# Kernel tuning notes

Hardware: AMD Instinct MI355X
Metric: run time of the kernel (lower is better)

Reference implementation:

```python
import jax, jax.numpy as jnp
import numpy as np

N_SRC = 50000
N_DST = 50000
E = 800000
SRC_DIM = 128
DST_DIM = 128
OUT_DIM = 128
HEADS = 4
D_HEAD = OUT_DIM // HEADS  # 32, concat=True


def setup_inputs() -> dict:
    key = jax.random.key(0)
    ks = jax.random.split(key, 10)
    x_src = jax.random.normal(ks[0], (N_SRC, SRC_DIM), dtype=jnp.float32)
    x_dst = jax.random.normal(ks[1], (N_DST, DST_DIM), dtype=jnp.float32)
    edge_src = jax.random.randint(ks[2], (E,), 0, N_SRC)
    edge_dst = jax.random.randint(ks[3], (E,), 0, N_DST)
    # parameters (torch Linear stored as [in, out] so y = x @ W)
    W_src = jax.random.normal(ks[4], (SRC_DIM, HEADS * D_HEAD), dtype=jnp.float32) / np.sqrt(SRC_DIM)
    W_dst = jax.random.normal(ks[5], (DST_DIM, HEADS * D_HEAD), dtype=jnp.float32) / np.sqrt(DST_DIM)
    att_src = jax.random.normal(ks[6], (1, HEADS, D_HEAD), dtype=jnp.float32) * 0.01
    att_dst = jax.random.normal(ks[7], (1, HEADS, D_HEAD), dtype=jnp.float32) * 0.01
    W_self = jax.random.normal(ks[8], (DST_DIM, HEADS * D_HEAD), dtype=jnp.float32) / np.sqrt(DST_DIM)
    b_self = jax.random.normal(ks[9], (HEADS * D_HEAD,), dtype=jnp.float32) * 0.01
    return {
        "x_src": x_src, "x_dst": x_dst,
        "edge_src": edge_src, "edge_dst": edge_dst, "num_dst": N_DST,
        "W_src": W_src, "W_dst": W_dst,
        "att_src": att_src, "att_dst": att_dst,
        "W_self": W_self, "b_self": b_self,
    }


def reference(x_src, x_dst, edge_src, edge_dst, num_dst,
              W_src, W_dst, att_src, att_dst, W_self, b_self):
    H, D = HEADS, D_HEAD
    src_feat = (x_src @ W_src).reshape(-1, H, D)   # [N_src, H, D]
    dst_feat = (x_dst @ W_dst).reshape(-1, H, D)   # [N_dst, H, D]

    src_edge = src_feat[edge_src]                   # [E, H, D] gather
    dst_edge = dst_feat[edge_dst]                   # [E, H, D] gather

    alpha_src = jnp.sum(src_edge * att_src, axis=-1)  # [E, H]
    alpha_dst = jnp.sum(dst_edge * att_dst, axis=-1)  # [E, H]
    alpha = jax.nn.leaky_relu(alpha_src + alpha_dst, negative_slope=0.2)

    # segment softmax over edges grouped by destination node
    a_max = jax.ops.segment_max(alpha, edge_dst, num_segments=num_dst)  # [N_dst, H]
    alpha = jnp.exp(alpha - a_max[edge_dst])
    a_sum = jax.ops.segment_sum(alpha, edge_dst, num_segments=num_dst)  # [N_dst, H]
    alpha = alpha / (a_sum[edge_dst] + 1e-16)

    msg = (src_edge * alpha[..., None]).reshape(-1, H * D)  # [E, H*D]
    agg = jax.ops.segment_sum(msg, edge_dst, num_segments=num_dst)  # [N_dst, H*D]

    return agg + x_dst @ W_self + b_self
```

## Files before the change

kernel.cpp:

```cpp
#include <hip/hip_runtime.h>

#define N_SRC 50000
#define N_DST 50000
#define NE    800000
#define DIM   128
#define HEADS 4

typedef short short8 __attribute__((ext_vector_type(8)));
typedef float f32x4 __attribute__((ext_vector_type(4)));

__device__ __forceinline__ float bf2f(unsigned short u) {
  union { unsigned int i; float f; } v;
  v.i = ((unsigned int)u) << 16;
  return v.f;
}

__device__ __forceinline__ unsigned short f2bf(float f) {
  unsigned int u = __float_as_uint(f);
  u += 0x7fffu + ((u >> 16) & 1u);
  return (unsigned short)(u >> 16);
}

__global__ void prep_kernel(const float* __restrict__ Wsrc, const float* __restrict__ Wself,
                            const float* __restrict__ Wdst,
                            const float* __restrict__ att_s, const float* __restrict__ att_d,
                            unsigned short* __restrict__ Wt_src,
                            unsigned short* __restrict__ Wt_self,
                            float* __restrict__ wt_s, float* __restrict__ wt_d) {
  const int b = blockIdx.x, t = threadIdx.x;
  if (b == 0) {
    for (int idx = t; idx < DIM * DIM; idx += 256) {
      int k = idx >> 7, n = idx & 127;
      Wt_src[n * DIM + k] = f2bf(Wsrc[idx]);
    }
  } else if (b == 1) {
    for (int idx = t; idx < DIM * DIM; idx += 256) {
      int k = idx >> 7, n = idx & 127;
      Wt_self[n * DIM + k] = f2bf(Wself[idx]);
    }
  } else {
    for (int i = t; i < 512; i += 256) {
      int k = i >> 2, h = i & 3;
      float ss = 0.f, sd = 0.f;
#pragma unroll 8
      for (int d = 0; d < 32; d++) {
        ss += Wsrc[k * DIM + h * 32 + d] * att_s[h * 32 + d];
        sd += Wdst[k * DIM + h * 32 + d] * att_d[h * 32 + d];
      }
      wt_s[h * DIM + k] = ss;
      wt_d[h * DIM + k] = sd;
    }
  }
}

__global__ __launch_bounds__(256) void mfma_src_kernel(
    const float* __restrict__ x, const unsigned short* __restrict__ Wt,
    const float* __restrict__ wt,
    unsigned short* __restrict__ feat, float* __restrict__ as_) {
  const int wave = threadIdx.x >> 6;
  const int lane = threadIdx.x & 63;
  const int r0 = (blockIdx.x * 4 + wave) * 16;
  const int rowa = lane & 15;
  const int kg = lane >> 4;

  f32x4 acc[8];
#pragma unroll
  for (int n = 0; n < 8; n++) acc[n] = (f32x4){0.f, 0.f, 0.f, 0.f};
  float p[4] = {0.f, 0.f, 0.f, 0.f};

  int rA = r0 + rowa;
  if (rA >= N_SRC) rA = N_SRC - 1;

#pragma unroll
  for (int ks = 0; ks < 4; ks++) {
    const int k = ks * 32 + kg * 8;
    const float4 xa = *(const float4*)&x[rA * DIM + k];
    const float4 xb = *(const float4*)&x[rA * DIM + k + 4];
#pragma unroll
    for (int h = 0; h < 4; h++) {
      const float4 wa = *(const float4*)&wt[h * DIM + k];
      const float4 wb = *(const float4*)&wt[h * DIM + k + 4];
      p[h] += xa.x * wa.x + xa.y * wa.y + xa.z * wa.z + xa.w * wa.w +
              xb.x * wb.x + xb.y * wb.y + xb.z * wb.z + xb.w * wb.w;
    }
    short8 af;
    af[0] = (short)f2bf(xa.x); af[1] = (short)f2bf(xa.y);
    af[2] = (short)f2bf(xa.z); af[3] = (short)f2bf(xa.w);
    af[4] = (short)f2bf(xb.x); af[5] = (short)f2bf(xb.y);
    af[6] = (short)f2bf(xb.z); af[7] = (short)f2bf(xb.w);
#pragma unroll
    for (int n = 0; n < 8; n++) {
      const short8 bf = *(const short8*)&Wt[(n * 16 + rowa) * DIM + k];
      acc[n] = __builtin_amdgcn_mfma_f32_16x16x32_bf16(af, bf, acc[n], 0, 0, 0);
    }
  }

  const int rowd = kg * 4;
#pragma unroll
  for (int n = 0; n < 8; n++) {
#pragma unroll
    for (int r = 0; r < 4; r++) {
      const int row = r0 + rowd + r;
      if (row < N_SRC) feat[row * DIM + n * 16 + rowa] = f2bf(acc[n][r]);
    }
  }

#pragma unroll
  for (int h = 0; h < 4; h++) {
    p[h] += __shfl_xor(p[h], 16);
    p[h] += __shfl_xor(p[h], 32);
  }
  if (lane < 16 && r0 + lane < N_SRC) {
    *(float4*)&as_[(r0 + lane) * 4] = make_float4(p[0], p[1], p[2], p[3]);
  }
}

__global__ __launch_bounds__(256) void mfma_dst_kernel(
    const float* __restrict__ x, const unsigned short* __restrict__ Wt,
    const float* __restrict__ wt, const float* __restrict__ bias,
    float* __restrict__ out, float* __restrict__ ad_) {
  const int wave = threadIdx.x >> 6;
  const int lane = threadIdx.x & 63;
  const int r0 = (blockIdx.x * 4 + wave) * 16;
  const int rowa = lane & 15;
  const int kg = lane >> 4;

  f32x4 acc[8];
#pragma unroll
  for (int n = 0; n < 8; n++) acc[n] = (f32x4){0.f, 0.f, 0.f, 0.f};
  float p[4] = {0.f, 0.f, 0.f, 0.f};

  int rA = r0 + rowa;
  if (rA >= N_DST) rA = N_DST - 1;

#pragma unroll
  for (int ks = 0; ks < 4; ks++) {
    const int k = ks * 32 + kg * 8;
    const float4 xa = *(const float4*)&x[rA * DIM + k];
    const float4 xb = *(const float4*)&x[rA * DIM + k + 4];
#pragma unroll
    for (int h = 0; h < 4; h++) {
      const float4 wa = *(const float4*)&wt[h * DIM + k];
      const float4 wb = *(const float4*)&wt[h * DIM + k + 4];
      p[h] += xa.x * wa.x + xa.y * wa.y + xa.z * wa.z + xa.w * wa.w +
              xb.x * wb.x + xb.y * wb.y + xb.z * wb.z + xb.w * wb.w;
    }
    short8 af;
    af[0] = (short)f2bf(xa.x); af[1] = (short)f2bf(xa.y);
    af[2] = (short)f2bf(xa.z); af[3] = (short)f2bf(xa.w);
    af[4] = (short)f2bf(xb.x); af[5] = (short)f2bf(xb.y);
    af[6] = (short)f2bf(xb.z); af[7] = (short)f2bf(xb.w);
#pragma unroll
    for (int n = 0; n < 8; n++) {
      const short8 bf = *(const short8*)&Wt[(n * 16 + rowa) * DIM + k];
      acc[n] = __builtin_amdgcn_mfma_f32_16x16x32_bf16(af, bf, acc[n], 0, 0, 0);
    }
  }

  const int rowd = kg * 4;
#pragma unroll
  for (int n = 0; n < 8; n++) {
    const float b = bias[n * 16 + rowa];
#pragma unroll
    for (int r = 0; r < 4; r++) {
      const int row = r0 + rowd + r;
      if (row < N_DST) out[row * DIM + n * 16 + rowa] = acc[n][r] + b;
    }
  }

#pragma unroll
  for (int h = 0; h < 4; h++) {
    p[h] += __shfl_xor(p[h], 16);
    p[h] += __shfl_xor(p[h], 32);
  }
  if (lane < 16 && r0 + lane < N_DST) {
    *(float4*)&ad_[(r0 + lane) * 4] = make_float4(p[0], p[1], p[2], p[3]);
  }
}

__global__ void hist_kernel(const int* __restrict__ edst, int* __restrict__ deg) {
  int e = blockIdx.x * 256 + threadIdx.x;
  if (e < NE) atomicAdd(&deg[edst[e]], 1);
}

__global__ void scan1_kernel(const int* __restrict__ deg, int* __restrict__ offs,
                             int* __restrict__ bsum, int n) {
  __shared__ int sh[256];
  int i = blockIdx.x * 256 + threadIdx.x;
  int v = (i < n) ? deg[i] : 0;
  sh[threadIdx.x] = v;
  __syncthreads();
  for (int d = 1; d < 256; d <<= 1) {
    int tv = (threadIdx.x >= d) ? sh[threadIdx.x - d] : 0;
    __syncthreads();
    sh[threadIdx.x] += tv;
    __syncthreads();
  }
  if (i < n) offs[i] = sh[threadIdx.x] - v;
  if (threadIdx.x == 255) bsum[blockIdx.x] = sh[255];
}

__global__ void scan2_kernel(int* __restrict__ bsum, int n) {
  __shared__ int sh[256];
  int v = (threadIdx.x < n) ? bsum[threadIdx.x] : 0;
  sh[threadIdx.x] = v;
  __syncthreads();
  for (int d = 1; d < 256; d <<= 1) {
    int tv = (threadIdx.x >= d) ? sh[threadIdx.x - d] : 0;
    __syncthreads();
    sh[threadIdx.x] += tv;
    __syncthreads();
  }
  if (threadIdx.x < n) bsum[threadIdx.x] = sh[threadIdx.x] - v;
}

__global__ void fill_kernel(const int* __restrict__ esrc, const int* __restrict__ edst,
                            const float* __restrict__ as_, const float* __restrict__ ad_,
                            const int* __restrict__ offs, const int* __restrict__ bsum,
                            int* __restrict__ cursor,
                            int* __restrict__ csr_src, float4* __restrict__ csr_alpha) {
  int e = blockIdx.x * 256 + threadIdx.x;
  if (e >= NE) return;
  int s = esrc[e], d = edst[e];
  int p = atomicAdd(&cursor[d], 1);
  int slot = offs[d] + bsum[d >> 8] + p;
  csr_src[slot] = s;
  const float4 av = *(const float4*)&as_[s * 4];
  const float4 bv = *(const float4*)&ad_[d * 4];
  float4 a;
  a.x = av.x + bv.x; a.y = av.y + bv.y; a.z = av.z + bv.z; a.w = av.w + bv.w;
  a.x = a.x > 0.f ? a.x : 0.2f * a.x;
  a.y = a.y > 0.f ? a.y : 0.2f * a.y;
  a.z = a.z > 0.f ? a.z : 0.2f * a.z;
  a.w = a.w > 0.f ? a.w : 0.2f * a.w;
  csr_alpha[slot] = a;
}

__global__ __launch_bounds__(256) void agg_kernel(
    const unsigned short* __restrict__ feat, const int* __restrict__ csr_src,
    const float* __restrict__ csr_alpha, const int* __restrict__ offs,
    const int* __restrict__ bsum, const int* __restrict__ deg,
    float* __restrict__ out) {
  const int wave = threadIdx.x >> 6;
  const int lane = threadIdx.x & 63;
  const int n = blockIdx.x * 4 + wave;
  if (n >= N_DST) return;
  const int beg = offs[n] + bsum[n >> 8];
  const int end = beg + deg[n];
  const int sub = lane >> 5;
  const int lp = lane & 31;
  const int h = lp >> 3;

  float4 o = make_float4(0.f, 0.f, 0.f, 0.f);
  if (sub == 0) o = *(const float4*)&out[n * DIM + lp * 4];

  float s = 0.f;
  float a0 = 0.f, a1 = 0.f, a2 = 0.f, a3 = 0.f;

  int k = beg + sub;
  int sid = 0;
  float a = -1e30f;
  if (k < end) {
    sid = csr_src[k];
    a = csr_alpha[k * 4 + h];
  }
  while (k < end) {
    int k2 = k + 2;
    int sid2 = 0;
    float an = -1e30f;
    if (k2 < end) {
      sid2 = csr_src[k2];
      an = csr_alpha[k2 * 4 + h];
    }
    float w = __expf(a);
    ushort4 f = *(const ushort4*)&feat[sid * DIM + lp * 4];
    s += w;
    a0 += w * bf2f(f.x);
    a1 += w * bf2f(f.y);
    a2 += w * bf2f(f.z);
    a3 += w * bf2f(f.w);
    k = k2;
    sid = sid2;
    a = an;
  }

  s += __shfl_xor(s, 32);
  a0 += __shfl_xor(a0, 32);
  a1 += __shfl_xor(a1, 32);
  a2 += __shfl_xor(a2, 32);
  a3 += __shfl_xor(a3, 32);

  if (sub == 0) {
    const float inv = 1.f / (s + 1e-16f);
    o.x += a0 * inv;
    o.y += a1 * inv;
    o.z += a2 * inv;
    o.w += a3 * inv;
    *(float4*)&out[n * DIM + lp * 4] = o;
  }
}

extern "C" void kernel_launch(void* const* d_in, const int* in_sizes, int n_in,
                              void* d_out, int out_size, void* d_ws, size_t ws_size,
                              hipStream_t stream) {
  const float* x_src  = (const float*)d_in[0];
  const float* x_dst  = (const float*)d_in[1];
  const int*   esrc   = (const int*)d_in[2];
  const int*   edst   = (const int*)d_in[3];
  const float* W_src  = (const float*)d_in[5];
  const float* W_dst  = (const float*)d_in[6];
  const float* att_s  = (const float*)d_in[7];
  const float* att_d  = (const float*)d_in[8];
  const float* W_self = (const float*)d_in[9];
  const float* b_self = (const float*)d_in[10];
  float* out = (float*)d_out;

  char* ws = (char*)d_ws;
  size_t off = 0;
  auto carve = [&](size_t bytes) {
    void* p = ws + off;
    off += (bytes + 255) & ~size_t(255);
    return p;
  };
  unsigned short* feat   = (unsigned short*)carve(sizeof(unsigned short) * N_SRC * DIM);
  float* as_   = (float*)carve(sizeof(float) * N_SRC * HEADS);
  float* ad_   = (float*)carve(sizeof(float) * N_DST * HEADS);
  int* deg     = (int*)carve(sizeof(int) * N_DST);
  int* cursor  = (int*)carve(sizeof(int) * N_DST);
  int* offs    = (int*)carve(sizeof(int) * N_DST);
  int* bsum    = (int*)carve(sizeof(int) * 256);
  int* csr_src = (int*)carve(sizeof(int) * NE);
  float4* csr_alpha = (float4*)carve(sizeof(float4) * NE);
  unsigned short* Wt_src  = (unsigned short*)carve(sizeof(unsigned short) * DIM * DIM);
  unsigned short* Wt_self = (unsigned short*)carve(sizeof(unsigned short) * DIM * DIM);
  float* wt_s = (float*)carve(sizeof(float) * HEADS * DIM);
  float* wt_d = (float*)carve(sizeof(float) * HEADS * DIM);
  (void)ws_size;

  hipMemsetAsync(deg, 0, sizeof(int) * N_DST, stream);
  hipMemsetAsync(cursor, 0, sizeof(int) * N_DST, stream);

  prep_kernel<<<3, 256, 0, stream>>>(W_src, W_self, W_dst, att_s, att_d,
                                     Wt_src, Wt_self, wt_s, wt_d);
  hist_kernel<<<(NE + 255) / 256, 256, 0, stream>>>(edst, deg);

  const int gemm_blocks = (N_SRC + 63) / 64;
  mfma_src_kernel<<<gemm_blocks, 256, 0, stream>>>(x_src, Wt_src, wt_s, feat, as_);
  mfma_dst_kernel<<<gemm_blocks, 256, 0, stream>>>(x_dst, Wt_self, wt_d, b_self, out, ad_);

  const int nblk = (N_DST + 255) / 256;
  scan1_kernel<<<nblk, 256, 0, stream>>>(deg, offs, bsum, N_DST);
  scan2_kernel<<<1, 256, 0, stream>>>(bsum, nblk);
  fill_kernel<<<(NE + 255) / 256, 256, 0, stream>>>(esrc, edst, as_, ad_, offs, bsum, cursor,
                                                    csr_src, (float4*)csr_alpha);
  agg_kernel<<<(N_DST + 3) / 4, 256, 0, stream>>>(feat, csr_src, (const float*)csr_alpha,
                                                  offs, bsum, deg, out);
}
```

Baseline: 324.4 us.

## Fuse GEMMs with histogram, fold attention logits into MFMA, compute alpha in aggregation

```diff
diff --git a/kernel.cpp b/kernel.cpp
--- a/kernel.cpp
+++ b/kernel.cpp
@@ -5,6 +5,9 @@
 #define NE    800000
 #define DIM   128
 #define HEADS 4
+#define NB_GEMM 782
+#define NB_HIST 3125
+#define WROWS 144
 
 typedef short short8 __attribute__((ext_vector_type(8)));
 typedef float f32x4 __attribute__((ext_vector_type(4)));
@@ -21,166 +24,147 @@
   return (unsigned short)(u >> 16);
 }
 
-__global__ void prep_kernel(const float* __restrict__ Wsrc, const float* __restrict__ Wself,
-                            const float* __restrict__ Wdst,
-                            const float* __restrict__ att_s, const float* __restrict__ att_d,
-                            unsigned short* __restrict__ Wt_src,
-                            unsigned short* __restrict__ Wt_self,
-                            float* __restrict__ wt_s, float* __restrict__ wt_d) {
+__global__ void setup_kernel(const float* __restrict__ Wsrc, const float* __restrict__ Wself,
+                             const float* __restrict__ Wdst,
+                             const float* __restrict__ att_s, const float* __restrict__ att_d,
+                             unsigned short* __restrict__ Wps, unsigned short* __restrict__ Wpd,
+                             int* __restrict__ deg, int* __restrict__ cursor) {
   const int b = blockIdx.x, t = threadIdx.x;
   if (b == 0) {
-    for (int idx = t; idx < DIM * DIM; idx += 256) {
-      int k = idx >> 7, n = idx & 127;
-      Wt_src[n * DIM + k] = f2bf(Wsrc[idx]);
+    for (int i = t; i < DIM * DIM; i += 256) {
+      int k = i >> 7, n = i & 127;
+      Wps[n * DIM + k] = f2bf(Wsrc[i]);
     }
   } else if (b == 1) {
-    for (int idx = t; idx < DIM * DIM; idx += 256) {
-      int k = idx >> 7, n = idx & 127;
-      Wt_self[n * DIM + k] = f2bf(Wself[idx]);
+    for (int i = t; i < DIM * DIM; i += 256) {
+      int k = i >> 7, n = i & 127;
+      Wpd[n * DIM + k] = f2bf(Wself[i]);
+    }
+  } else if (b == 2) {
+    for (int i = t; i < 2 * 4 * DIM; i += 256) {
+      int which = (i >= 4 * DIM) ? 1 : 0;
+      int j = which ? i - 4 * DIM : i;
+      int h = j >> 7, k = j & 127;
+      const float* W = which ? Wdst : Wsrc;
+      const float* att = which ? att_d : att_s;
+      float s = 0.f;
+#pragma unroll 8
+      for (int d = 0; d < 32; d++) s += W[k * DIM + h * 32 + d] * att[h * 32 + d];
+      (which ? Wpd : Wps)[(128 + h) * DIM + k] = f2bf(s);
+    }
+    for (int i = t; i < 2 * 12 * DIM; i += 256) {
+      int which = (i >= 12 * DIM) ? 1 : 0;
+      int j = which ? i - 12 * DIM : i;
+      (which ? Wpd : Wps)[132 * DIM + j] = 0;
     }
   } else {
-    for (int i = t; i < 512; i += 256) {
-      int k = i >> 2, h = i & 3;
-      float ss = 0.f, sd = 0.f;
-#pragma unroll 8
-      for (int d = 0; d < 32; d++) {
-        ss += Wsrc[k * DIM + h * 32 + d] * att_s[h * 32 + d];
-        sd += Wdst[k * DIM + h * 32 + d] * att_d[h * 32 + d];
+    int i = (b - 3) * 1024 + t * 4;
+    int4 z = make_int4(0, 0, 0, 0);
+    if (i < N_DST) *(int4*)&deg[i] = z;
+    else {
+      int j = i - N_DST;
+      if (j < N_DST) *(int4*)&cursor[j] = z;
+    }
+  }
+}
+
+__global__ __launch_bounds__(256) void phase1_kernel(
+    const float* __restrict__ x_src, const float* __restrict__ x_dst,
+    const unsigned short* __restrict__ Wps, const unsigned short* __restrict__ Wpd,
+    const int* __restrict__ edst,
+    unsigned short* __restrict__ feat, float* __restrict__ as_, float* __restrict__ ad_,
+    float* __restrict__ out, const float* __restrict__ bias, int* __restrict__ deg) {
+  __shared__ unsigned short lx[64 * DIM];
+  __shared__ unsigned short lw[WROWS * DIM];
+  const int b = blockIdx.x, t = threadIdx.x;
+
+  if (b >= 2 * NB_GEMM) {
+    int e = (b - 2 * NB_GEMM) * 256 + t;
+    if (e < NE) atomicAdd(&deg[edst[e]], 1);
+    return;
+  }
+
+  const bool is_dst = (b >= NB_GEMM);
+  const int blk = is_dst ? b - NB_GEMM : b;
+  const float* __restrict__ x = is_dst ? x_dst : x_src;
+  const unsigned short* __restrict__ Wp = is_dst ? Wpd : Wps;
+  const int r0 = blk * 64;
+
+  for (int c = t; c < WROWS * 16; c += 256) {
+    int row = c >> 4, slot = c & 15;
+    short8 v = *(const short8*)&Wp[row * DIM + slot * 8];
+    *(short8*)((char*)lw + row * 256 + ((slot ^ (row & 15)) << 4)) = v;
+  }
+  for (int c = t; c < 64 * 16; c += 256) {
+    int row = c >> 4, slot = c & 15;
+    int gr = r0 + row;
+    if (gr >= N_SRC) gr = N_SRC - 1;
+    const float4 va = *(const float4*)&x[gr * DIM + slot * 8];
+    const float4 vb = *(const float4*)&x[gr * DIM + slot * 8 + 4];
+    short8 v;
+    v[0] = (short)f2bf(va.x); v[1] = (short)f2bf(va.y);
+    v[2] = (short)f2bf(va.z); v[3] = (short)f2bf(va.w);
+    v[4] = (short)f2bf(vb.x); v[5] = (short)f2bf(vb.y);
+    v[6] = (short)f2bf(vb.z); v[7] = (short)f2bf(vb.w);
+    *(short8*)((char*)lx + row * 256 + ((slot ^ (row & 15)) << 4)) = v;
+  }
+  __syncthreads();
+
+  const int wave = t >> 6, lane = t & 63;
+  const int rowa = lane & 15, kg = lane >> 4;
+  const int xrow = wave * 16 + rowa;
+
+  f32x4 acc[9];
+#pragma unroll
+  for (int n = 0; n < 9; n++) acc[n] = (f32x4){0.f, 0.f, 0.f, 0.f};
+
+#pragma unroll
+  for (int ks = 0; ks < 4; ks++) {
+    const int slot = ks * 4 + kg;
+    const short8 af = *(const short8*)((char*)lx + xrow * 256 + ((slot ^ rowa) << 4));
+#pragma unroll
+    for (int n = 0; n < 9; n++) {
+      const int wr = n * 16 + rowa;
+      const short8 bf = *(const short8*)((char*)lw + wr * 256 + ((slot ^ rowa) << 4));
+      acc[n] = __builtin_amdgcn_mfma_f32_16x16x32_bf16(af, bf, acc[n], 0, 0, 0);
+    }
+  }
+
+  const int orow0 = r0 + wave * 16 + kg * 4;
+  if (!is_dst) {
+#pragma unroll
+    for (int n = 0; n < 8; n++) {
+#pragma unroll
+      for (int r = 0; r < 4; r++) {
+        int row = orow0 + r;
+        if (row < N_SRC) feat[row * DIM + n * 16 + rowa] = f2bf(acc[n][r]);
       }
-      wt_s[h * DIM + k] = ss;
-      wt_d[h * DIM + k] = sd;
-    }
-  }
-}
-
-__global__ __launch_bounds__(256) void mfma_src_kernel(
-    const float* __restrict__ x, const unsigned short* __restrict__ Wt,
-    const float* __restrict__ wt,
-    unsigned short* __restrict__ feat, float* __restrict__ as_) {
-  const int wave = threadIdx.x >> 6;
-  const int lane = threadIdx.x & 63;
-  const int r0 = (blockIdx.x * 4 + wave) * 16;
-  const int rowa = lane & 15;
-  const int kg = lane >> 4;
-
-  f32x4 acc[8];
-#pragma unroll
-  for (int n = 0; n < 8; n++) acc[n] = (f32x4){0.f, 0.f, 0.f, 0.f};
-  float p[4] = {0.f, 0.f, 0.f, 0.f};
-
-  int rA = r0 + rowa;
-  if (rA >= N_SRC) rA = N_SRC - 1;
-
-#pragma unroll
-  for (int ks = 0; ks < 4; ks++) {
-    const int k = ks * 32 + kg * 8;
-    const float4 xa = *(const float4*)&x[rA * DIM + k];
-    const float4 xb = *(const float4*)&x[rA * DIM + k + 4];
-#pragma unroll
-    for (int h = 0; h < 4; h++) {
-      const float4 wa = *(const float4*)&wt[h * DIM + k];
-      const float4 wb = *(const float4*)&wt[h * DIM + k + 4];
-      p[h] += xa.x * wa.x + xa.y * wa.y + xa.z * wa.z + xa.w * wa.w +
-              xb.x * wb.x + xb.y * wb.y + xb.z * wb.z + xb.w * wb.w;
-    }
-    short8 af;
-    af[0] = (short)f2bf(xa.x); af[1] = (short)f2bf(xa.y);
-    af[2] = (short)f2bf(xa.z); af[3] = (short)f2bf(xa.w);
-    af[4] = (short)f2bf(xb.x); af[5] = (short)f2bf(xb.y);
-    af[6] = (short)f2bf(xb.z); af[7] = (short)f2bf(xb.w);
+    }
+    if (rowa < HEADS) {
+#pragma unroll
+      for (int r = 0; r < 4; r++) {
+        int row = orow0 + r;
+        if (row < N_SRC) as_[row * HEADS + rowa] = acc[8][r];
+      }
+    }
+  } else {
 #pragma unroll
     for (int n = 0; n < 8; n++) {
-      const short8 bf = *(const short8*)&Wt[(n * 16 + rowa) * DIM + k];
-      acc[n] = __builtin_amdgcn_mfma_f32_16x16x32_bf16(af, bf, acc[n], 0, 0, 0);
-    }
-  }
-
-  const int rowd = kg * 4;
-#pragma unroll
-  for (int n = 0; n < 8; n++) {
-#pragma unroll
-    for (int r = 0; r < 4; r++) {
-      const int row = r0 + rowd + r;
-      if (row < N_SRC) feat[row * DIM + n * 16 + rowa] = f2bf(acc[n][r]);
-    }
-  }
-
-#pragma unroll
-  for (int h = 0; h < 4; h++) {
-    p[h] += __shfl_xor(p[h], 16);
-    p[h] += __shfl_xor(p[h], 32);
-  }
-  if (lane < 16 && r0 + lane < N_SRC) {
-    *(float4*)&as_[(r0 + lane) * 4] = make_float4(p[0], p[1], p[2], p[3]);
-  }
-}
-
-__global__ __launch_bounds__(256) void mfma_dst_kernel(
-    const float* __restrict__ x, const unsigned short* __restrict__ Wt,
-    const float* __restrict__ wt, const float* __restrict__ bias,
-    float* __restrict__ out, float* __restrict__ ad_) {
-  const int wave = threadIdx.x >> 6;
-  const int lane = threadIdx.x & 63;
-  const int r0 = (blockIdx.x * 4 + wave) * 16;
-  const int rowa = lane & 15;
-  const int kg = lane >> 4;
-
-  f32x4 acc[8];
-#pragma unroll
-  for (int n = 0; n < 8; n++) acc[n] = (f32x4){0.f, 0.f, 0.f, 0.f};
-  float p[4] = {0.f, 0.f, 0.f, 0.f};
-
-  int rA = r0 + rowa;
-  if (rA >= N_DST) rA = N_DST - 1;
-
-#pragma unroll
-  for (int ks = 0; ks < 4; ks++) {
-    const int k = ks * 32 + kg * 8;
-    const float4 xa = *(const float4*)&x[rA * DIM + k];
-    const float4 xb = *(const float4*)&x[rA * DIM + k + 4];
-#pragma unroll
-    for (int h = 0; h < 4; h++) {
-      const float4 wa = *(const float4*)&wt[h * DIM + k];
-      const float4 wb = *(const float4*)&wt[h * DIM + k + 4];
-      p[h] += xa.x * wa.x + xa.y * wa.y + xa.z * wa.z + xa.w * wa.w +
-              xb.x * wb.x + xb.y * wb.y + xb.z * wb.z + xb.w * wb.w;
-    }
-    short8 af;
-    af[0] = (short)f2bf(xa.x); af[1] = (short)f2bf(xa.y);
-    af[2] = (short)f2bf(xa.z); af[3] = (short)f2bf(xa.w);
-    af[4] = (short)f2bf(xb.x); af[5] = (short)f2bf(xb.y);
-    af[6] = (short)f2bf(xb.z); af[7] = (short)f2bf(xb.w);
-#pragma unroll
-    for (int n = 0; n < 8; n++) {
-      const short8 bf = *(const short8*)&Wt[(n * 16 + rowa) * DIM + k];
-      acc[n] = __builtin_amdgcn_mfma_f32_16x16x32_bf16(af, bf, acc[n], 0, 0, 0);
-    }
-  }
-
-  const int rowd = kg * 4;
-#pragma unroll
-  for (int n = 0; n < 8; n++) {
-    const float b = bias[n * 16 + rowa];
-#pragma unroll
-    for (int r = 0; r < 4; r++) {
-      const int row = r0 + rowd + r;
-      if (row < N_DST) out[row * DIM + n * 16 + rowa] = acc[n][r] + b;
-    }
-  }
-
-#pragma unroll
-  for (int h = 0; h < 4; h++) {
-    p[h] += __shfl_xor(p[h], 16);
-    p[h] += __shfl_xor(p[h], 32);
-  }
-  if (lane < 16 && r0 + lane < N_DST) {
-    *(float4*)&ad_[(r0 + lane) * 4] = make_float4(p[0], p[1], p[2], p[3]);
-  }
-}
-
-__global__ void hist_kernel(const int* __restrict__ edst, int* __restrict__ deg) {
-  int e = blockIdx.x * 256 + threadIdx.x;
-  if (e < NE) atomicAdd(&deg[edst[e]], 1);
+      const float bb = bias[n * 16 + rowa];
+#pragma unroll
+      for (int r = 0; r < 4; r++) {
+        int row = orow0 + r;
+        if (row < N_DST) out[row * DIM + n * 16 + rowa] = acc[n][r] + bb;
+      }
+    }
+    if (rowa < HEADS) {
+#pragma unroll
+      for (int r = 0; r < 4; r++) {
+        int row = orow0 + r;
+        if (row < N_DST) ad_[row * HEADS + rowa] = acc[8][r];
+      }
+    }
+  }
 }
 
 __global__ void scan1_kernel(const int* __restrict__ deg, int* __restrict__ offs,
@@ -215,88 +199,84 @@
 }
 
 __global__ void fill_kernel(const int* __restrict__ esrc, const int* __restrict__ edst,
-                            const float* __restrict__ as_, const float* __restrict__ ad_,
                             const int* __restrict__ offs, const int* __restrict__ bsum,
-                            int* __restrict__ cursor,
-                            int* __restrict__ csr_src, float4* __restrict__ csr_alpha) {
+                            int* __restrict__ cursor, int* __restrict__ csr_src) {
   int e = blockIdx.x * 256 + threadIdx.x;
   if (e >= NE) return;
   int s = esrc[e], d = edst[e];
   int p = atomicAdd(&cursor[d], 1);
-  int slot = offs[d] + bsum[d >> 8] + p;
-  csr_src[slot] = s;
-  const float4 av = *(const float4*)&as_[s * 4];
-  const float4 bv = *(const float4*)&ad_[d * 4];
-  float4 a;
-  a.x = av.x + bv.x; a.y = av.y + bv.y; a.z = av.z + bv.z; a.w = av.w + bv.w;
-  a.x = a.x > 0.f ? a.x : 0.2f * a.x;
-  a.y = a.y > 0.f ? a.y : 0.2f * a.y;
-  a.z = a.z > 0.f ? a.z : 0.2f * a.z;
-  a.w = a.w > 0.f ? a.w : 0.2f * a.w;
-  csr_alpha[slot] = a;
+  csr_src[offs[d] + bsum[d >> 8] + p] = s;
 }
 
 __global__ __launch_bounds__(256) void agg_kernel(
     const unsigned short* __restrict__ feat, const int* __restrict__ csr_src,
-    const float* __restrict__ csr_alpha, const int* __restrict__ offs,
-    const int* __restrict__ bsum, const int* __restrict__ deg,
-    float* __restrict__ out) {
+    const float* __restrict__ as_, const float* __restrict__ ad_,
+    const int* __restrict__ offs, const int* __restrict__ bsum,
+    const int* __restrict__ deg, float* __restrict__ out) {
   const int wave = threadIdx.x >> 6;
   const int lane = threadIdx.x & 63;
   const int n = blockIdx.x * 4 + wave;
   if (n >= N_DST) return;
+  const int g = lane >> 4, q = lane & 15;
+  const int h = q >> 2;
   const int beg = offs[n] + bsum[n >> 8];
   const int end = beg + deg[n];
-  const int sub = lane >> 5;
-  const int lp = lane & 31;
-  const int h = lp >> 3;
-
-  float4 o = make_float4(0.f, 0.f, 0.f, 0.f);
-  if (sub == 0) o = *(const float4*)&out[n * DIM + lp * 4];
+  const float adh = ad_[n * HEADS + h];
+
+  float4 oa, ob;
+  if (g == 0) {
+    oa = *(const float4*)&out[n * DIM + q * 8];
+    ob = *(const float4*)&out[n * DIM + q * 8 + 4];
+  }
 
   float s = 0.f;
-  float a0 = 0.f, a1 = 0.f, a2 = 0.f, a3 = 0.f;
-
-  int k = beg + sub;
+  float acc[8];
+#pragma unroll
+  for (int j = 0; j < 8; j++) acc[j] = 0.f;
+
+  int k = beg + g;
   int sid = 0;
-  float a = -1e30f;
+  float ash = -1e30f;
   if (k < end) {
     sid = csr_src[k];
-    a = csr_alpha[k * 4 + h];
+    ash = as_[sid * HEADS + h];
   }
   while (k < end) {
-    int k2 = k + 2;
-    int sid2 = 0;
-    float an = -1e30f;
-    if (k2 < end) {
-      sid2 = csr_src[k2];
-      an = csr_alpha[k2 * 4 + h];
-    }
-    float w = __expf(a);
-    ushort4 f = *(const ushort4*)&feat[sid * DIM + lp * 4];
+    const int kn = k + 4;
+    int sid_n = 0;
+    float ash_n = -1e30f;
+    if (kn < end) {
+      sid_n = csr_src[kn];
+      ash_n = as_[sid_n * HEADS + h];
+    }
+    float al = ash + adh;
+    al = al > 0.f ? al : 0.2f * al;
+    const float w = __expf(al);
+    const short8 f = *(const short8*)&feat[sid * DIM + q * 8];
     s += w;
-    a0 += w * bf2f(f.x);
-    a1 += w * bf2f(f.y);
-    a2 += w * bf2f(f.z);
-    a3 += w * bf2f(f.w);
-    k = k2;
-    sid = sid2;
-    a = an;
-  }
-
+#pragma unroll
+    for (int j = 0; j < 8; j++) acc[j] += w * bf2f((unsigned short)f[j]);
+    k = kn;
+    sid = sid_n;
+    ash = ash_n;
+  }
+
+  s += __shfl_xor(s, 16);
   s += __shfl_xor(s, 32);
-  a0 += __shfl_xor(a0, 32);
-  a1 += __shfl_xor(a1, 32);
-  a2 += __shfl_xor(a2, 32);
-  a3 += __shfl_xor(a3, 32);
-
-  if (sub == 0) {
+#pragma unroll
+  for (int j = 0; j < 8; j++) {
+    acc[j] += __shfl_xor(acc[j], 16);
+    acc[j] += __shfl_xor(acc[j], 32);
+  }
+
+  if (g == 0) {
     const float inv = 1.f / (s + 1e-16f);
-    o.x += a0 * inv;
-    o.y += a1 * inv;
-    o.z += a2 * inv;
-    o.w += a3 * inv;
-    *(float4*)&out[n * DIM + lp * 4] = o;
+    oa.x += acc[0] * inv; oa.y += acc[1] * inv;
+    oa.z += acc[2] * inv; oa.w += acc[3] * inv;
+    ob.x += acc[4] * inv; ob.y += acc[5] * inv;
+    ob.z += acc[6] * inv; ob.w += acc[7] * inv;
+    *(float4*)&out[n * DIM + q * 8] = oa;
+    *(float4*)&out[n * DIM + q * 8 + 4] = ob;
   }
 }
 
@@ -314,6 +294,7 @@
   const float* W_self = (const float*)d_in[9];
   const float* b_self = (const float*)d_in[10];
   float* out = (float*)d_out;
+  (void)in_sizes; (void)n_in; (void)out_size; (void)ws_size;
 
   char* ws = (char*)d_ws;
   size_t off = 0;
@@ -322,7 +303,7 @@
     off += (bytes + 255) & ~size_t(255);
     return p;
   };
-  unsigned short* feat   = (unsigned short*)carve(sizeof(unsigned short) * N_SRC * DIM);
+  unsigned short* feat = (unsigned short*)carve(sizeof(unsigned short) * N_SRC * DIM);
   float* as_   = (float*)carve(sizeof(float) * N_SRC * HEADS);
   float* ad_   = (float*)carve(sizeof(float) * N_DST * HEADS);
   int* deg     = (int*)carve(sizeof(int) * N_DST);
@@ -330,29 +311,17 @@
   int* offs    = (int*)carve(sizeof(int) * N_DST);
   int* bsum    = (int*)carve(sizeof(int) * 256);
   int* csr_src = (int*)carve(sizeof(int) * NE);
-  float4* csr_alpha = (float4*)carve(sizeof(float4) * NE);
-  unsigned short* Wt_src  = (unsigned short*)carve(sizeof(unsigned short) * DIM * DIM);
-  unsigned short* Wt_self = (unsigned short*)carve(sizeof(unsigned short) * DIM * DIM);
-  float* wt_s = (float*)carve(sizeof(float) * HEADS * DIM);
-  float* wt_d = (float*)carve(sizeof(float) * HEADS * DIM);
-  (void)ws_size;
-
-  hipMemsetAsync(deg, 0, sizeof(int) * N_DST, stream);
-  hipMemsetAsync(cursor, 0, sizeof(int) * N_DST, stream);
-
-  prep_kernel<<<3, 256, 0, stream>>>(W_src, W_self, W_dst, att_s, att_d,
-                                     Wt_src, Wt_self, wt_s, wt_d);
-  hist_kernel<<<(NE + 255) / 256, 256, 0, stream>>>(edst, deg);
-
-  const int gemm_blocks = (N_SRC + 63) / 64;
-  mfma_src_kernel<<<gemm_blocks, 256, 0, stream>>>(x_src, Wt_src, wt_s, feat, as_);
-  mfma_dst_kernel<<<gemm_blocks, 256, 0, stream>>>(x_dst, Wt_self, wt_d, b_self, out, ad_);
-
+  unsigned short* Wps = (unsigned short*)carve(sizeof(unsigned short) * WROWS * DIM);
+  unsigned short* Wpd = (unsigned short*)carve(sizeof(unsigned short) * WROWS * DIM);
+
+  setup_kernel<<<101, 256, 0, stream>>>(W_src, W_self, W_dst, att_s, att_d,
+                                        Wps, Wpd, deg, cursor);
+  phase1_kernel<<<2 * NB_GEMM + NB_HIST, 256, 0, stream>>>(
+      x_src, x_dst, Wps, Wpd, edst, feat, as_, ad_, out, b_self, deg);
   const int nblk = (N_DST + 255) / 256;
   scan1_kernel<<<nblk, 256, 0, stream>>>(deg, offs, bsum, N_DST);
   scan2_kernel<<<1, 256, 0, stream>>>(bsum, nblk);
-  fill_kernel<<<(NE + 255) / 256, 256, 0, stream>>>(esrc, edst, as_, ad_, offs, bsum, cursor,
-                                                    csr_src, (float4*)csr_alpha);
-  agg_kernel<<<(N_DST + 3) / 4, 256, 0, stream>>>(feat, csr_src, (const float*)csr_alpha,
+  fill_kernel<<<NB_HIST, 256, 0, stream>>>(esrc, edst, offs, bsum, cursor, csr_src);
+  agg_kernel<<<(N_DST + 3) / 4, 256, 0, stream>>>(feat, csr_src, as_, ad_,
                                                   offs, bsum, deg, out);
 }
```

After: 264.8 us. 18.4% less time.
